# Optimization experiments

Hardware: AMD Instinct MI355X
Metric: run time of the kernel (lower is better)

The kernel has to match this reference:

```python
import jax, jax.numpy as jnp
import numpy as np
import math

N_NODES = 50000
N_EDGES = 800000
IN_DIM = 128
HID = 128
OUT_DIM = 2048
N_LABEL_EDGES = 4096
POOL_RATIO = 0.5
NUM_HEADS = 8


def seg_sum(x, idx, n):
    return jax.ops.segment_sum(x, idx, num_segments=n)


def graph_conv(x, W, b, src, dst, emask, n):
    # DGL GraphConv, norm='both': D_out^-1/2 A D_in^-1/2 (x W) + b (masked edges)
    deg_out = seg_sum(emask, src, n)
    deg_in = seg_sum(emask, dst, n)
    ns = jax.lax.rsqrt(jnp.maximum(deg_out, 1.0))
    nd = jax.lax.rsqrt(jnp.maximum(deg_in, 1.0))
    h = x @ W
    msg = (h * ns[:, None])[src] * emask[:, None]
    agg = seg_sum(msg, dst, n)
    return agg * nd[:, None] + b


def conv_pool_block(x, src, dst, emask, cW, cb, sW, sb):
    # GraphConv -> ReLU -> SAGPool(top-k by GraphConv score, tanh gate) -> avg||max readout
    n = x.shape[0]
    h = jax.nn.relu(graph_conv(x, cW, cb, src, dst, emask, n))
    score = graph_conv(h, sW, sb, src, dst, emask, n)[:, 0]
    k = int(math.ceil(POOL_RATIO * n))  # static
    _, perm = jax.lax.top_k(score, k)
    h_new = h[perm] * jnp.tanh(score[perm])[:, None]
    # remap edges to the pooled node set; drop edges touching removed nodes via mask
    newid = jnp.full((n,), -1, jnp.int32).at[perm].set(jnp.arange(k, dtype=jnp.int32))
    nsrc = newid[src]
    ndst = newid[dst]
    new_mask = emask * (nsrc >= 0).astype(emask.dtype) * (ndst >= 0).astype(emask.dtype)
    nsrc = jnp.maximum(nsrc, 0)
    ndst = jnp.maximum(ndst, 0)
    readout = jnp.concatenate([h_new.mean(0), h_new.max(0)])[None, :]  # [1, 2*HID]
    return h_new, nsrc, ndst, new_mask, readout


def gat_conv(x, fcW, al, ar, lsrc, ldst, n, slope=0.2):
    # GATConv(1 -> 1, num_heads=8): head feature dim is 1
    h = x @ fcW                      # [n, heads]
    el = h * al
    er = h * ar
    e = jax.nn.leaky_relu(el[lsrc] + er[ldst], slope)  # [E_l, heads]
    emax = jax.ops.segment_max(e, ldst, num_segments=n)
    emax = jnp.where(jnp.isfinite(emax), emax, 0.0)
    ex = jnp.exp(e - emax[ldst])
    denom = seg_sum(ex, ldst, n)
    alpha = ex / jnp.maximum(denom[ldst], 1e-9)
    out = seg_sum(alpha * h[lsrc], ldst, n)            # [n, heads]
    return out[:, :, None]                             # [n, heads, 1]


def setup_inputs() -> dict:
    key = jax.random.key(0)
    ks = jax.random.split(key, 32)

    def rn(k, shape, s=0.05):
        return jax.random.normal(k, shape, jnp.float32) * s

    inp = {}
    inp['feat'] = jax.random.normal(ks[0], (N_NODES, IN_DIM), jnp.float32)
    inp['sequence_feature'] = jax.random.normal(ks[1], (1, 1024), jnp.float32)
    inp['src'] = jax.random.randint(ks[2], (N_EDGES,), 0, N_NODES, jnp.int32)
    inp['dst'] = jax.random.randint(ks[3], (N_EDGES,), 0, N_NODES, jnp.int32)
    inp['label_src'] = jax.random.randint(ks[4], (N_LABEL_EDGES,), 0, OUT_DIM, jnp.int32)
    inp['label_dst'] = jax.random.randint(ks[5], (N_LABEL_EDGES,), 0, OUT_DIM, jnp.int32)
    i = 6
    for b in range(3):
        din = IN_DIM if b == 0 else HID
        inp['cW%d' % b] = rn(ks[i], (din, HID)); i += 1
        inp['cb%d' % b] = jnp.zeros((HID,), jnp.float32)
        inp['sW%d' % b] = rn(ks[i], (HID, 1)); i += 1
        inp['sb%d' % b] = jnp.zeros((1,), jnp.float32)
    inp['lin1W'] = rn(ks[i], (2 * HID + 1024, 2 * HID)); i += 1
    inp['lin1b'] = jnp.zeros((2 * HID,), jnp.float32)
    inp['lin2W'] = rn(ks[i], (2 * HID, HID)); i += 1
    inp['lin2b'] = jnp.zeros((HID,), jnp.float32)
    inp['lin3W'] = rn(ks[i], (HID, OUT_DIM)); i += 1
    inp['lin3b'] = jnp.zeros((OUT_DIM,), jnp.float32)
    inp['gat_fcW'] = rn(ks[i], (1, NUM_HEADS)); i += 1
    inp['gat_al'] = rn(ks[i], (NUM_HEADS,)); i += 1
    inp['gat_ar'] = rn(ks[i], (NUM_HEADS,)); i += 1
    return inp


def reference(feat, sequence_feature, src, dst, label_src, label_dst,
              cW0, cb0, sW0, sb0, cW1, cb1, sW1, sb1, cW2, cb2, sW2, sb2,
              lin1W, lin1b, lin2W, lin2b, lin3W, lin3b,
              gat_fcW, gat_al, gat_ar):
    x, s, d = feat, src, dst
    emask = jnp.ones((src.shape[0],), jnp.float32)
    final = None
    for cW, cb, sW, sb in ((cW0, cb0, sW0, sb0), (cW1, cb1, sW1, sb1), (cW2, cb2, sW2, sb2)):
        x, s, d, emask, ro = conv_pool_block(x, s, d, emask, cW, cb, sW, sb)
        final = ro if final is None else final + ro
    final = jnp.concatenate([final, sequence_feature], axis=-1)  # [1, 2*HID+1024]
    f = jax.nn.relu(final @ lin1W + lin1b)
    # dropout: eval mode -> identity
    f = jax.nn.relu(f @ lin2W + lin2b)
    f = f @ lin3W + lin3b          # [1, OUT_DIM]
    ft = f.T                       # [OUT_DIM, 1]
    gat_out = gat_conv(ft, gat_fcW, gat_al, gat_ar, label_src, label_dst, OUT_DIM)
    max_value = jnp.max(gat_out, axis=1)      # [OUT_DIM, 1]
    _ = ft - jax.nn.relu(max_value)           # computed then discarded, as in source
    return ft.T
```

## Files before the change

kernel.cpp:

```cpp
#include <hip/hip_runtime.h>
#include <hip/hip_bf16.h>
#include <cmath>

#define N0 50000
#define NEDGE 800000
#define NEG_HUGE -3.402823466e38f
#define STRIDE 128

typedef int i32x4 __attribute__((ext_vector_type(4)));
typedef __attribute__((ext_vector_type(8))) short short8v;
typedef __attribute__((ext_vector_type(4))) float f32x4;

__device__ inline float b2f(unsigned short u) { return __uint_as_float(((unsigned)u) << 16); }

__device__ inline unsigned short f2b(float f) {
    __hip_bfloat16 h = __float2bfloat16(f);
    return *(unsigned short*)&h;
}

__device__ inline unsigned fkey(float f) {
    unsigned b = __float_as_uint(f);
    if (b == 0x80000000u) b = 0u;
    return (b & 0x80000000u) ? ~b : (b | 0x80000000u);
}

__device__ inline void atomicMaxF(float* a, float v) {
    if (v >= 0.f) atomicMax((int*)a, __float_as_int(v));
    else          atomicMin((unsigned int*)a, __float_as_uint(v));
}

__global__ void k_init(float* finalv, int* deg_out, int* fill,
                       int* binsA, int* binsB, float* maxbuf, int* ctrl) {
    int i = blockIdx.x * blockDim.x + threadIdx.x;
    if (i < 256) finalv[i] = 0.f;
    if (i < 384) maxbuf[i] = NEG_HUGE;
    if (i < N0) { deg_out[i] = 0; fill[i] = 0; }
    if (i < 65536) { binsA[i] = 0; binsB[i] = 0; }
    if (i < 2) ctrl[8 + i] = 0;
}

__global__ __launch_bounds__(256) void k_build(
        const int* __restrict__ esrc, const int* __restrict__ edst,
        int* deg_out, int* fill, int* csr_src) {
    int t = blockIdx.x * 256 + threadIdx.x;
    int e0 = t * 4;
    if (e0 >= NEDGE) return;
    i32x4 a = __builtin_nontemporal_load((const i32x4*)(esrc + e0));
    i32x4 bq = __builtin_nontemporal_load((const i32x4*)(edst + e0));
    int s[4] = {a.x, a.y, a.z, a.w};
    int d[4] = {bq.x, bq.y, bq.z, bq.w};
#pragma unroll
    for (int kq = 0; kq < 4; ++kq) {
        atomicAdd(&deg_out[s[kq]], 1);
        int pos = atomicAdd(&fill[d[kq]], 1);
        if (pos < STRIDE) csr_src[(size_t)d[kq] * STRIDE + pos] = s[kq];
    }
}

__global__ __launch_bounds__(256) void k_rmbuild(
        const int* __restrict__ esrc, const int* __restrict__ edst,
        const int2* __restrict__ ein, int use_pair,
        const int* __restrict__ ctrl, int slot,
        const int* __restrict__ newid,
        int2* __restrict__ eout, int* __restrict__ outcnt,
        int* deg_out, int* fill, int* csr_src) {
    __shared__ int wbase[4];
    __shared__ int blkbase;
    int E = (slot < 0) ? NEDGE : ctrl[slot];
    if (blockIdx.x * 256 >= E) return;
    int i = blockIdx.x * 256 + threadIdx.x;
    int lane = threadIdx.x & 63, w = threadIdx.x >> 6;
    int ns = -1, nd = -1;
    if (i < E) {
        int s, d;
        if (use_pair) { int2 pr = ein[i]; s = pr.x; d = pr.y; }
        else { s = esrc[i]; d = edst[i]; }
        ns = newid[s]; nd = newid[d];
    }
    bool keep = (ns >= 0) && (nd >= 0);
    unsigned long long m = __ballot(keep);
    int rank = __popcll(m & ((1ull << lane) - 1ull));
    if (lane == 0) wbase[w] = __popcll(m);
    __syncthreads();
    if (threadIdx.x == 0)
        blkbase = atomicAdd(outcnt, wbase[0] + wbase[1] + wbase[2] + wbase[3]);
    __syncthreads();
    int base = blkbase;
    for (int q = 0; q < w; ++q) base += wbase[q];
    if (keep) {
        eout[base + rank] = make_int2(ns, nd);
        atomicAdd(&deg_out[ns], 1);
        int pos = atomicAdd(&fill[nd], 1);
        if (pos < STRIDE) csr_src[(size_t)nd * STRIDE + pos] = ns;
    }
}

__global__ __launch_bounds__(256) void k_gemm(
        const float* __restrict__ feat, const float* __restrict__ xprev,
        const int* __restrict__ oldid, const float* __restrict__ garr,
        const int* __restrict__ deg_out,
        const float* __restrict__ W, unsigned short* __restrict__ hpre,
        int n, int nprev, int mode) {
    __shared__ short Wt[128][136];
    __shared__ short Xt[64][136];
    __shared__ int ridx_s[64];
    __shared__ float esc_s[64];
    int tid = threadIdx.x;
    int r0 = blockIdx.x * 64;
    if (tid < 64) {
        int gr = r0 + tid;
        int ridx = 0; float esc = 0.f;
        if (gr < n) {
            if (mode == 0) {
                ridx = gr;
                esc = rsqrtf(fmaxf((float)deg_out[gr], 1.f));
            } else {
                int orow = oldid[gr];
                if ((unsigned)orow < (unsigned)nprev) {
                    ridx = orow;
                    esc = rsqrtf(fmaxf((float)deg_out[gr], 1.f)) * garr[gr];
                }
            }
        }
        ridx_s[tid] = ridx;
        esc_s[tid] = esc;
    }
    __syncthreads();
    {
        int col = tid & 127;
        int kh = tid >> 7;
#pragma unroll
        for (int c8 = 0; c8 < 8; ++c8) {
            int kb = kh * 64 + c8 * 8;
            unsigned short v[8];
#pragma unroll
            for (int j = 0; j < 8; ++j)
                v[j] = f2b(W[(size_t)(kb + j) * 128 + col]);
            *(uint4*)&Wt[col][kb] = *(uint4*)v;
        }
    }
    {
        const float* xsrc = (mode == 0) ? feat : xprev;
        int rr = tid >> 2;
        int kx = (tid & 3) * 32;
        const float4* xp = (const float4*)(xsrc + (size_t)ridx_s[rr] * 128 + kx);
#pragma unroll
        for (int c4 = 0; c4 < 8; ++c4) {
            float4 v = xp[c4];
            unsigned short u[4];
            u[0] = f2b(v.x); u[1] = f2b(v.y); u[2] = f2b(v.z); u[3] = f2b(v.w);
            *(uint2*)&Xt[rr][kx + c4 * 4] = *(uint2*)u;
        }
    }
    __syncthreads();

    int lane = tid & 63, w = tid >> 6;
    int row16 = lane & 15;
    int ko = (lane >> 4) * 8;
    f32x4 acc[8];
#pragma unroll
    for (int t = 0; t < 8; ++t) acc[t] = (f32x4){0.f, 0.f, 0.f, 0.f};
#pragma unroll
    for (int kc = 0; kc < 4; ++kc) {
        int kbase = kc * 32 + ko;
        short8v a = *(short8v*)&Xt[w * 16 + row16][kbase];
#pragma unroll
        for (int t = 0; t < 8; ++t) {
            short8v b = *(short8v*)&Wt[t * 16 + row16][kbase];
            acc[t] = __builtin_amdgcn_mfma_f32_16x16x32_bf16(a, b, acc[t], 0, 0, 0);
        }
    }
    int rq = (lane >> 4) * 4;
    float esc[4];
#pragma unroll
    for (int r = 0; r < 4; ++r) esc[r] = esc_s[w * 16 + rq + r];
#pragma unroll
    for (int r = 0; r < 4; ++r) {
        int gr = r0 + w * 16 + rq + r;
        if (gr < n) {
            unsigned short* op = hpre + (size_t)gr * 128;
#pragma unroll
            for (int t = 0; t < 8; ++t)
                op[t * 16 + (lane & 15)] = f2b(acc[t][r] * esc[r]);
        }
    }
}

__global__ __launch_bounds__(256) void k_agg_conv(
        const unsigned short* __restrict__ hpre, const int* __restrict__ fill,
        const int* __restrict__ deg_out,
        const int* __restrict__ csr_src,
        const float* __restrict__ cb, const float* __restrict__ sW,
        float* __restrict__ hpost, float* __restrict__ hs, int n) {
    int wid = threadIdx.x >> 6;
    int lane = threadIdx.x & 63;
    int d = blockIdx.x * 4 + wid;
    if (d >= n) return;
    int degin = fill[d];
    int cnt = min(degin, STRIDE);
    const int* bp = csr_src + (size_t)d * STRIDE;
    float a0 = 0.f, a1 = 0.f;
    int j = 0;
    for (; j + 8 <= cnt; j += 8) {
        int4 s0 = *(const int4*)(bp + j);
        int4 s1 = *(const int4*)(bp + j + 4);
        ushort2 u0 = ((const ushort2*)(hpre + (size_t)s0.x * 128))[lane];
        ushort2 u1 = ((const ushort2*)(hpre + (size_t)s0.y * 128))[lane];
        ushort2 u2 = ((const ushort2*)(hpre + (size_t)s0.z * 128))[lane];
        ushort2 u3 = ((const ushort2*)(hpre + (size_t)s0.w * 128))[lane];
        ushort2 u4 = ((const ushort2*)(hpre + (size_t)s1.x * 128))[lane];
        ushort2 u5 = ((const ushort2*)(hpre + (size_t)s1.y * 128))[lane];
        ushort2 u6 = ((const ushort2*)(hpre + (size_t)s1.z * 128))[lane];
        ushort2 u7 = ((const ushort2*)(hpre + (size_t)s1.w * 128))[lane];
        a0 += ((b2f(u0.x) + b2f(u1.x)) + (b2f(u2.x) + b2f(u3.x))) +
              ((b2f(u4.x) + b2f(u5.x)) + (b2f(u6.x) + b2f(u7.x)));
        a1 += ((b2f(u0.y) + b2f(u1.y)) + (b2f(u2.y) + b2f(u3.y))) +
              ((b2f(u4.y) + b2f(u5.y)) + (b2f(u6.y) + b2f(u7.y)));
    }
    for (; j + 4 <= cnt; j += 4) {
        int4 ss = *(const int4*)(bp + j);
        ushort2 u0 = ((const ushort2*)(hpre + (size_t)ss.x * 128))[lane];
        ushort2 u1 = ((const ushort2*)(hpre + (size_t)ss.y * 128))[lane];
        ushort2 u2 = ((const ushort2*)(hpre + (size_t)ss.z * 128))[lane];
        ushort2 u3 = ((const ushort2*)(hpre + (size_t)ss.w * 128))[lane];
        a0 += (b2f(u0.x) + b2f(u1.x)) + (b2f(u2.x) + b2f(u3.x));
        a1 += (b2f(u0.y) + b2f(u1.y)) + (b2f(u2.y) + b2f(u3.y));
    }
    for (; j < cnt; ++j) {
        int s0 = bp[j];
        ushort2 u0 = ((const ushort2*)(hpre + (size_t)s0 * 128))[lane];
        a0 += b2f(u0.x);
        a1 += b2f(u0.y);
    }
    float nd2 = rsqrtf(fmaxf((float)degin, 1.f));
    int c0 = lane * 2;
    float h0 = fmaxf(fmaf(a0, nd2, cb[c0]), 0.f);
    float h1 = fmaxf(fmaf(a1, nd2, cb[c0 + 1]), 0.f);
    ((float2*)(hpost + (size_t)d * 128))[lane] = make_float2(h0, h1);
    float v = h0 * sW[c0] + h1 * sW[c0 + 1];
#pragma unroll
    for (int off = 32; off; off >>= 1) v += __shfl_down(v, off);
    if (lane == 0) hs[d] = v * rsqrtf(fmaxf((float)deg_out[d], 1.f));
}

__global__ void k_score_hist(const float* __restrict__ hs, const int* __restrict__ fill,
                             const int* __restrict__ csr_src,
                             const float* __restrict__ sb, float* score,
                             int* binsA, int n) {
    int d = blockIdx.x * blockDim.x + threadIdx.x;
    if (d >= n) return;
    int degin = fill[d];
    int cnt = min(degin, STRIDE);
    const int* bp = csr_src + (size_t)d * STRIDE;
    float sum = 0.f;
    int j = 0;
    for (; j + 8 <= cnt; j += 8) {
        int4 s0 = *(const int4*)(bp + j);
        int4 s1 = *(const int4*)(bp + j + 4);
        sum += ((hs[s0.x] + hs[s0.y]) + (hs[s0.z] + hs[s0.w])) +
               ((hs[s1.x] + hs[s1.y]) + (hs[s1.z] + hs[s1.w]));
    }
    for (; j + 4 <= cnt; j += 4) {
        int4 ss = *(const int4*)(bp + j);
        sum += (hs[ss.x] + hs[ss.y]) + (hs[ss.z] + hs[ss.w]);
    }
    for (; j < cnt; ++j) sum += hs[bp[j]];
    float sc = rsqrtf(fmaxf((float)degin, 1.f)) * sum + sb[0];
    score[d] = sc;
    atomicAdd(&binsA[fkey(sc) >> 16], 1);
}

__global__ void k_rhist2(const float* __restrict__ score, const int* __restrict__ ctrl,
                         int n, int* binsB) {
    unsigned p16 = (unsigned)ctrl[3];
    for (int i = blockIdx.x * 256 + threadIdx.x; i < n; i += gridDim.x * 256) {
        unsigned u = fkey(score[i]);
        if ((u >> 16) == p16) atomicAdd(&binsB[u & 0xFFFFu], 1);
    }
}

__global__ void k_rpick(int stage, int k0, int* ctrl, const int* __restrict__ bins) {
    __shared__ int gs[64];
    __shared__ int arr[1024];
    __shared__ int wsum[16];
    __shared__ int sChunk, sKrem;
    int t = threadIdx.x;
    {
        int c = t >> 4, sub = t & 15;
        const int4* p4 = (const int4*)(bins + (size_t)c * 1024);
        int s = 0;
#pragma unroll
        for (int q = 0; q < 16; ++q) {
            int4 v = p4[q * 16 + sub];
            s += v.x + v.y + v.z + v.w;
        }
#pragma unroll
        for (int off = 8; off; off >>= 1) s += __shfl_down(s, off, 16);
        if (sub == 0) gs[c] = s;
    }
    __syncthreads();
    if (t == 0) {
        int kneed = (stage == 0) ? k0 : ctrl[4];
        int cum = 0, c = 63;
        for (; c >= 1; --c) { int v = gs[c]; if (cum + v >= kneed) break; cum += v; }
        sChunk = c; sKrem = kneed - cum;
    }
    __syncthreads();
    int c = sChunk;
    int v = bins[(size_t)c * 1024 + t];
    arr[t] = v;
    int lane = t & 63, w = t >> 6;
    int s = v;
#pragma unroll
    for (int off = 32; off; off >>= 1) s += __shfl_down(s, off);
    if (lane == 0) wsum[w] = s;
    __syncthreads();
    if (t == 0) {
        int kneed = sKrem;
        int cum = 0, w2 = 15;
        for (; w2 >= 1; --w2) { int vv = wsum[w2]; if (cum + vv >= kneed) break; cum += vv; }
        int j = 63;
        for (; j >= 1; --j) { int vv = arr[w2 * 64 + j]; if (cum + vv >= kneed) break; cum += vv; }
        int bin = c * 1024 + w2 * 64 + j;
        if (stage == 0) { ctrl[3] = bin; ctrl[4] = kneed - cum; }
        else {
            ctrl[0] = (int)((((unsigned)ctrl[3]) << 16) | (unsigned)bin);
            ctrl[2] = kneed - cum;
        }
    }
}

__global__ __launch_bounds__(1024) void k_cemit2(
        const float* __restrict__ score, const int* __restrict__ ctrl,
        int n, int knext, int* newid, int* oldid, float* garr,
        int* deg_out, int* fill, int* binsA, int* binsB,
        const float* __restrict__ hpost, float* finalv, float* maxbuf, float invk) {
    __shared__ int wG[16], wE[16];
    __shared__ int redCG[16], redCE[16];
    __shared__ int selIdx[1024];
    __shared__ float selG[1024];
    __shared__ int selCnt;
    __shared__ float redS[1024], redM[1024];
    int b = blockIdx.x, tid = threadIdx.x;
    int lane = tid & 63, wv = tid >> 6;
    unsigned T = (unsigned)ctrl[0];
    int needEq = ctrl[2];

    if (knext > 0) {
        int gt = b * 1024 + tid, nt = gridDim.x * 1024;
        for (int z = gt; z < 65536; z += nt) { binsA[z] = 0; binsB[z] = 0; }
        for (int z = gt; z < knext; z += nt) { deg_out[z] = 0; fill[z] = 0; }
    }

    int cg_ = 0, ce_ = 0;
    int end = b << 10;
    for (int i = tid; i < end; i += 1024) {
        unsigned u = fkey(score[i]);
        cg_ += (u > T);
        ce_ += (u == T);
    }
#pragma unroll
    for (int off = 32; off; off >>= 1) {
        cg_ += __shfl_down(cg_, off);
        ce_ += __shfl_down(ce_, off);
    }
    if (lane == 0) { redCG[wv] = cg_; redCE[wv] = ce_; }
    if (tid == 0) selCnt = 0;

    int i = (b << 10) + tid;
    bool inb = (i < n);
    float sc = inb ? score[i] : 0.f;
    unsigned u = inb ? fkey(sc) : 0u;
    bool isG = inb && (u > T);
    bool isE = inb && (u == T);
    unsigned long long mG = __ballot(isG);
    unsigned long long mE = __ballot(isE);
    if (lane == 0) { wG[wv] = __popcll(mG); wE[wv] = __popcll(mE); }
    __syncthreads();

    int sGoff = 0, sEoff = 0;
#pragma unroll
    for (int w = 0; w < 16; ++w) { sGoff += redCG[w]; sEoff += redCE[w]; }
    int gW = 0, eW = 0;
    for (int w = 0; w < wv; ++w) { gW += wG[w]; eW += wE[w]; }
    unsigned long long below = (1ull << lane) - 1ull;
    int Gb = sGoff + gW + __popcll(mG & below);
    int Eb = sEoff + eW + __popcll(mE & below);
    if (inb) {
        bool sel = isG || (isE && (Eb < needEq));
        if (sel) {
            int j = Gb + min(Eb, needEq);
            newid[i] = j;
            oldid[j] = i;
            float g = tanhf(sc);
            garr[j] = g;
            int p = atomicAdd(&selCnt, 1);
            selIdx[p] = i;
            selG[p] = g;
        } else {
            newid[i] = -1;
        }
    }
    __syncthreads();

    int m = selCnt;
    int grp = tid >> 7, c = tid & 127;
    float sum = 0.f, mx = NEG_HUGE;
    for (int r = grp; r < m; r += 8) {
        float v = hpost[(size_t)selIdx[r] * 128 + c] * selG[r];
        sum += v;
        mx = fmaxf(mx, v);
    }
    redS[tid] = sum;
    redM[tid] = mx;
    __syncthreads();
    if (tid < 128) {
        float s2 = 0.f, m2 = NEG_HUGE;
#pragma unroll
        for (int g2 = 0; g2 < 8; ++g2) {
            s2 += redS[g2 * 128 + tid];
            m2 = fmaxf(m2, redM[g2 * 128 + tid]);
        }
        atomicAdd(&finalv[tid], s2 * invk);
        atomicMaxF(&maxbuf[tid], m2);
    }
}

__global__ __launch_bounds__(1024) void k_mlp(
        const float* __restrict__ finalv, const float* __restrict__ maxbuf,
        const float* __restrict__ seq,
        const float* __restrict__ W1, const float* __restrict__ b1,
        const float* __restrict__ W2, const float* __restrict__ b2,
        const float* __restrict__ W3, const float* __restrict__ b3,
        float* out) {
    __shared__ float fv[1280];
    __shared__ float part[1024];
    __shared__ float f1s[256];
    __shared__ float f2s[128];
    int tid = threadIdx.x;
    for (int j = tid; j < 1280; j += 1024) {
        float v;
        if (j < 128) v = finalv[j];
        else if (j < 256) v = maxbuf[j - 128] + maxbuf[j] + maxbuf[j + 128];
        else v = seq[j - 256];
        fv[j] = v;
    }
    __syncthreads();
    {
        int o = tid & 255, pr = tid >> 8;
        float acc = 0.f;
        for (int j = pr * 320; j < (pr + 1) * 320; ++j)
            acc = fmaf(fv[j], W1[(size_t)j * 256 + o], acc);
        part[tid] = acc;
    }
    __syncthreads();
    if (tid < 256) {
        float a = part[tid] + part[tid + 256] + part[tid + 512] + part[tid + 768];
        f1s[tid] = fmaxf(a + b1[tid], 0.f);
    }
    __syncthreads();
    {
        int o = tid & 127, pr = tid >> 7;
        float acc = 0.f;
        for (int j = pr * 32; j < (pr + 1) * 32; ++j)
            acc = fmaf(f1s[j], W2[(size_t)j * 128 + o], acc);
        part[tid] = acc;
    }
    __syncthreads();
    if (tid < 128) {
        float a = 0.f;
#pragma unroll
        for (int q = 0; q < 8; ++q) a += part[q * 128 + tid];
        f2s[tid] = fmaxf(a + b2[tid], 0.f);
    }
    __syncthreads();
    for (int col = tid; col < 2048; col += 1024) {
        float acc = 0.f;
#pragma unroll 4
        for (int j = 0; j < 128; ++j)
            acc = fmaf(f2s[j], W3[(size_t)j * 2048 + col], acc);
        out[col] = acc + b3[col];
    }
}

extern "C" void kernel_launch(void* const* d_in, const int* in_sizes, int n_in,
                              void* d_out, int out_size, void* d_ws, size_t ws_size,
                              hipStream_t stream) {
    (void)in_sizes; (void)n_in; (void)out_size; (void)ws_size;
    const float* feat = (const float*)d_in[0];
    const float* seq  = (const float*)d_in[1];
    const int* src = (const int*)d_in[2];
    const int* dst = (const int*)d_in[3];
    const float *cW[3], *cb[3], *sW[3], *sb[3];
    for (int b = 0; b < 3; ++b) {
        cW[b] = (const float*)d_in[6 + 4 * b];
        cb[b] = (const float*)d_in[7 + 4 * b];
        sW[b] = (const float*)d_in[8 + 4 * b];
        sb[b] = (const float*)d_in[9 + 4 * b];
    }
    const float* lin1W = (const float*)d_in[18];
    const float* lin1b = (const float*)d_in[19];
    const float* lin2W = (const float*)d_in[20];
    const float* lin2b = (const float*)d_in[21];
    const float* lin3W = (const float*)d_in[22];
    const float* lin3b = (const float*)d_in[23];
    float* out = (float*)d_out;

    char* p = (char*)d_ws;
    size_t off = 0;
    auto alloc = [&](size_t bytes) -> void* {
        void* r = p + off;
        off = (off + bytes + 255) & ~(size_t)255;
        return r;
    };
    unsigned short* hpre = (unsigned short*)alloc((size_t)N0 * 128 * 2);
    float* hpost  = (float*)alloc((size_t)N0 * 128 * 4);
    float* hs     = (float*)alloc((size_t)N0 * 4);
    float* score  = (float*)alloc((size_t)N0 * 4);
    int* deg_out  = (int*)alloc((size_t)N0 * 4);
    int* fill     = (int*)alloc((size_t)N0 * 4);
    int2* epair1  = (int2*)alloc((size_t)NEDGE * 8);
    int* csr_src  = (int*)alloc((size_t)N0 * STRIDE * 4);
    int* newid    = (int*)alloc((size_t)N0 * 4);
    int* oldid    = (int*)alloc((size_t)25000 * 4);
    float* garr   = (float*)alloc((size_t)25000 * 4);
    float* maxbuf = (float*)alloc(3 * 128 * 4);
    float* finalv = (float*)alloc(256 * 4);
    int* ctrl     = (int*)alloc(64 * 4);
    int* binsA    = (int*)alloc(65536 * 4);
    int* binsB    = (int*)alloc(65536 * 4);
    int2* epair2  = (int2*)hpre;

    const int nb[3] = {50000, 25000, 12500};
    const int kb[3] = {25000, 12500, 6250};

    k_init<<<256, 256, 0, stream>>>(finalv, deg_out, fill, binsA, binsB, maxbuf, ctrl);

    for (int b = 0; b < 3; ++b) {
        int n = nb[b], k = kb[b];
        int B = (n + 1023) / 1024;
        if (b == 0)
            k_build<<<(NEDGE / 4 + 255) / 256, 256, 0, stream>>>(src, dst, deg_out, fill,
                                                                 csr_src);
        else if (b == 1)
            k_rmbuild<<<(NEDGE + 255) / 256, 256, 0, stream>>>(
                src, dst, (const int2*)0, 0, ctrl, -1, newid, epair1, ctrl + 8,
                deg_out, fill, csr_src);
        else
            k_rmbuild<<<(NEDGE + 255) / 256, 256, 0, stream>>>(
                (const int*)0, (const int*)0, epair1, 1, ctrl, 8, newid, epair2, ctrl + 9,
                deg_out, fill, csr_src);
        k_gemm<<<(n + 63) / 64, 256, 0, stream>>>(feat, hpost, oldid, garr, deg_out, cW[b],
                                                  hpre, n, (b > 0) ? nb[b - 1] : 1,
                                                  (b == 0) ? 0 : 1);
        k_agg_conv<<<(n + 3) / 4, 256, 0, stream>>>(hpre, fill, deg_out, csr_src, cb[b],
                                                    sW[b], hpost, hs, n);
        k_score_hist<<<(n + 255) / 256, 256, 0, stream>>>(hs, fill, csr_src, sb[b],
                                                          score, binsA, n);
        k_rpick<<<1, 1024, 0, stream>>>(0, k, ctrl, binsA);
        k_rhist2<<<128, 256, 0, stream>>>(score, ctrl, n, binsB);
        k_rpick<<<1, 1024, 0, stream>>>(1, k, ctrl, binsB);
        k_cemit2<<<B, 1024, 0, stream>>>(score, ctrl, n, (b < 2) ? kb[b] : 0,
                                         newid, oldid, garr, deg_out, fill, binsA, binsB,
                                         hpost, finalv, maxbuf + b * 128,
                                         1.0f / (float)k);
    }

    k_mlp<<<1, 1024, 0, stream>>>(finalv, maxbuf, seq, lin1W, lin1b, lin2W, lin2b,
                                  lin3W, lin3b, out);
}
```

Measured before the change: 597.4 us.

## Compute out-degree via LDS histograms and widen aggregation gathers to 8-byte loads

```diff
diff --git a/kernel.cpp b/kernel.cpp
--- a/kernel.cpp
+++ b/kernel.cpp
@@ -6,6 +6,8 @@
 #define NEDGE 800000
 #define NEG_HUGE -3.402823466e38f
 #define STRIDE 128
+#define HBINS 12500
+#define HSLICE 16
 
 typedef int i32x4 __attribute__((ext_vector_type(4)));
 typedef __attribute__((ext_vector_type(8))) short short8v;
@@ -39,9 +41,42 @@
     if (i < 2) ctrl[8 + i] = 0;
 }
 
+__global__ __launch_bounds__(1024) void k_hist(const int* __restrict__ esrc,
+                                               unsigned* __restrict__ deg_part) {
+    __shared__ unsigned hist[HBINS];
+    int b = blockIdx.x;
+    int r = b & 3;
+    int slice = b >> 2;
+    for (int i = threadIdx.x; i < HBINS; i += 1024) hist[i] = 0;
+    __syncthreads();
+    int lo = r * HBINS;
+    int base = slice * (NEDGE / HSLICE);
+    for (int e = threadIdx.x * 4; e < NEDGE / HSLICE; e += 4096) {
+        i32x4 a = __builtin_nontemporal_load((const i32x4*)(esrc + base + e));
+        int ss[4] = {a.x, a.y, a.z, a.w};
+#pragma unroll
+        for (int q = 0; q < 4; ++q) {
+            unsigned loc = (unsigned)(ss[q] - lo);
+            if (loc < (unsigned)HBINS) atomicAdd(&hist[loc], 1u);
+        }
+    }
+    __syncthreads();
+    for (int i = threadIdx.x; i < HBINS; i += 1024)
+        deg_part[(size_t)slice * N0 + lo + i] = hist[i];
+}
+
+__global__ void k_dsum(const unsigned* __restrict__ deg_part, int* deg_out) {
+    int v = blockIdx.x * 256 + threadIdx.x;
+    if (v >= N0) return;
+    unsigned s = 0;
+#pragma unroll
+    for (int q = 0; q < HSLICE; ++q) s += deg_part[(size_t)q * N0 + v];
+    deg_out[v] = (int)s;
+}
+
 __global__ __launch_bounds__(256) void k_build(
         const int* __restrict__ esrc, const int* __restrict__ edst,
-        int* deg_out, int* fill, int* csr_src) {
+        int* fill, int* csr_src) {
     int t = blockIdx.x * 256 + threadIdx.x;
     int e0 = t * 4;
     if (e0 >= NEDGE) return;
@@ -51,7 +86,6 @@
     int d[4] = {bq.x, bq.y, bq.z, bq.w};
 #pragma unroll
     for (int kq = 0; kq < 4; ++kq) {
-        atomicAdd(&deg_out[s[kq]], 1);
         int pos = atomicAdd(&fill[d[kq]], 1);
         if (pos < STRIDE) csr_src[(size_t)d[kq] * STRIDE + pos] = s[kq];
     }
@@ -199,47 +233,47 @@
     int degin = fill[d];
     int cnt = min(degin, STRIDE);
     const int* bp = csr_src + (size_t)d * STRIDE;
-    float a0 = 0.f, a1 = 0.f;
+    int half = lane >> 5;
+    int l32 = lane & 31;
+    float a0 = 0.f, a1 = 0.f, a2 = 0.f, a3 = 0.f;
     int j = 0;
     for (; j + 8 <= cnt; j += 8) {
-        int4 s0 = *(const int4*)(bp + j);
-        int4 s1 = *(const int4*)(bp + j + 4);
-        ushort2 u0 = ((const ushort2*)(hpre + (size_t)s0.x * 128))[lane];
-        ushort2 u1 = ((const ushort2*)(hpre + (size_t)s0.y * 128))[lane];
-        ushort2 u2 = ((const ushort2*)(hpre + (size_t)s0.z * 128))[lane];
-        ushort2 u3 = ((const ushort2*)(hpre + (size_t)s0.w * 128))[lane];
-        ushort2 u4 = ((const ushort2*)(hpre + (size_t)s1.x * 128))[lane];
-        ushort2 u5 = ((const ushort2*)(hpre + (size_t)s1.y * 128))[lane];
-        ushort2 u6 = ((const ushort2*)(hpre + (size_t)s1.z * 128))[lane];
-        ushort2 u7 = ((const ushort2*)(hpre + (size_t)s1.w * 128))[lane];
-        a0 += ((b2f(u0.x) + b2f(u1.x)) + (b2f(u2.x) + b2f(u3.x))) +
-              ((b2f(u4.x) + b2f(u5.x)) + (b2f(u6.x) + b2f(u7.x)));
-        a1 += ((b2f(u0.y) + b2f(u1.y)) + (b2f(u2.y) + b2f(u3.y))) +
-              ((b2f(u4.y) + b2f(u5.y)) + (b2f(u6.y) + b2f(u7.y)));
-    }
-    for (; j + 4 <= cnt; j += 4) {
-        int4 ss = *(const int4*)(bp + j);
-        ushort2 u0 = ((const ushort2*)(hpre + (size_t)ss.x * 128))[lane];
-        ushort2 u1 = ((const ushort2*)(hpre + (size_t)ss.y * 128))[lane];
-        ushort2 u2 = ((const ushort2*)(hpre + (size_t)ss.z * 128))[lane];
-        ushort2 u3 = ((const ushort2*)(hpre + (size_t)ss.w * 128))[lane];
+        int s0 = bp[j + half];
+        int s1 = bp[j + 2 + half];
+        int s2 = bp[j + 4 + half];
+        int s3 = bp[j + 6 + half];
+        ushort4 u0 = ((const ushort4*)(hpre + (size_t)s0 * 128))[l32];
+        ushort4 u1 = ((const ushort4*)(hpre + (size_t)s1 * 128))[l32];
+        ushort4 u2 = ((const ushort4*)(hpre + (size_t)s2 * 128))[l32];
+        ushort4 u3 = ((const ushort4*)(hpre + (size_t)s3 * 128))[l32];
         a0 += (b2f(u0.x) + b2f(u1.x)) + (b2f(u2.x) + b2f(u3.x));
         a1 += (b2f(u0.y) + b2f(u1.y)) + (b2f(u2.y) + b2f(u3.y));
-    }
-    for (; j < cnt; ++j) {
-        int s0 = bp[j];
-        ushort2 u0 = ((const ushort2*)(hpre + (size_t)s0 * 128))[lane];
-        a0 += b2f(u0.x);
-        a1 += b2f(u0.y);
-    }
+        a2 += (b2f(u0.z) + b2f(u1.z)) + (b2f(u2.z) + b2f(u3.z));
+        a3 += (b2f(u0.w) + b2f(u1.w)) + (b2f(u2.w) + b2f(u3.w));
+    }
+    for (; j < cnt; j += 2) {
+        int jj = j + half;
+        if (jj < cnt) {
+            int s0 = bp[jj];
+            ushort4 u0 = ((const ushort4*)(hpre + (size_t)s0 * 128))[l32];
+            a0 += b2f(u0.x); a1 += b2f(u0.y); a2 += b2f(u0.z); a3 += b2f(u0.w);
+        }
+    }
+    a0 += __shfl_xor(a0, 32);
+    a1 += __shfl_xor(a1, 32);
+    a2 += __shfl_xor(a2, 32);
+    a3 += __shfl_xor(a3, 32);
     float nd2 = rsqrtf(fmaxf((float)degin, 1.f));
-    int c0 = lane * 2;
+    int c0 = l32 * 4;
     float h0 = fmaxf(fmaf(a0, nd2, cb[c0]), 0.f);
     float h1 = fmaxf(fmaf(a1, nd2, cb[c0 + 1]), 0.f);
-    ((float2*)(hpost + (size_t)d * 128))[lane] = make_float2(h0, h1);
-    float v = h0 * sW[c0] + h1 * sW[c0 + 1];
-#pragma unroll
-    for (int off = 32; off; off >>= 1) v += __shfl_down(v, off);
+    float h2 = fmaxf(fmaf(a2, nd2, cb[c0 + 2]), 0.f);
+    float h3 = fmaxf(fmaf(a3, nd2, cb[c0 + 3]), 0.f);
+    if (half == 0)
+        ((float4*)(hpost + (size_t)d * 128))[l32] = make_float4(h0, h1, h2, h3);
+    float v = h0 * sW[c0] + h1 * sW[c0 + 1] + h2 * sW[c0 + 2] + h3 * sW[c0 + 3];
+#pragma unroll
+    for (int off = 16; off; off >>= 1) v += __shfl_down(v, off);
     if (lane == 0) hs[d] = v * rsqrtf(fmaxf((float)deg_out[d], 1.f));
 }
 
@@ -519,6 +553,7 @@
     float* score  = (float*)alloc((size_t)N0 * 4);
     int* deg_out  = (int*)alloc((size_t)N0 * 4);
     int* fill     = (int*)alloc((size_t)N0 * 4);
+    unsigned* deg_part = (unsigned*)alloc((size_t)HSLICE * N0 * 4);
     int2* epair1  = (int2*)alloc((size_t)NEDGE * 8);
     int* csr_src  = (int*)alloc((size_t)N0 * STRIDE * 4);
     int* newid    = (int*)alloc((size_t)N0 * 4);
@@ -539,17 +574,19 @@
     for (int b = 0; b < 3; ++b) {
         int n = nb[b], k = kb[b];
         int B = (n + 1023) / 1024;
-        if (b == 0)
-            k_build<<<(NEDGE / 4 + 255) / 256, 256, 0, stream>>>(src, dst, deg_out, fill,
-                                                                 csr_src);
-        else if (b == 1)
+        if (b == 0) {
+            k_hist<<<64, 1024, 0, stream>>>(src, deg_part);
+            k_dsum<<<(N0 + 255) / 256, 256, 0, stream>>>(deg_part, deg_out);
+            k_build<<<(NEDGE / 4 + 255) / 256, 256, 0, stream>>>(src, dst, fill, csr_src);
+        } else if (b == 1) {
             k_rmbuild<<<(NEDGE + 255) / 256, 256, 0, stream>>>(
                 src, dst, (const int2*)0, 0, ctrl, -1, newid, epair1, ctrl + 8,
                 deg_out, fill, csr_src);
-        else
+        } else {
             k_rmbuild<<<(NEDGE + 255) / 256, 256, 0, stream>>>(
                 (const int*)0, (const int*)0, epair1, 1, ctrl, 8, newid, epair2, ctrl + 9,
                 deg_out, fill, csr_src);
+        }
         k_gemm<<<(n + 63) / 64, 256, 0, stream>>>(feat, hpost, oldid, garr, deg_out, cW[b],
                                                   hpre, n, (b > 0) ? nb[b - 1] : 1,
                                                   (b == 0) ? 0 : 1);
```

Result: faster. 582.0 us (-2.6%).
